# Performance work log

Hardware: AMD Instinct MI355X
Metric: run time of the kernel (lower is better)

Reference implementation:

```python
import jax, jax.numpy as jnp
import numpy as np

V = 131072        # vocab size = number of leaves (power of 2)
D = 17            # tree depth = log2(V)
B = 16384
E = 128


def setup_inputs() -> dict:
    key = jax.random.key(0)
    k1, k2, k3 = jax.random.split(key, 3)
    embeddings = jax.random.normal(k1, (B, E), dtype=jnp.float32)
    word_idx = jax.random.randint(k2, (B,), 0, V)
    # one Linear(E, 1) per internal node of the complete binary tree: V-1 internal nodes
    W = jax.random.normal(k3, (V - 1, E), dtype=jnp.float32) * (1.0 / np.sqrt(E))
    b = jnp.zeros((V - 1,), dtype=jnp.float32)
    return {"embeddings": embeddings, "word_idx": word_idx, "W": W, "b": b}


def _paths(word_idx):
    # Heap layout: leaf for word w is at index V-1+w; parent(i) = (i-1)//2.
    # Left child (2p+1, odd index) subtree holds the smaller words -> target 1.
    node = word_idx + (V - 1)
    nodes, dirs = [], []
    for _ in range(D):  # fixed small depth loop, unrolled by jit
        parent = (node - 1) // 2
        nodes.append(parent)
        dirs.append(node % 2)  # 1 iff we came from the left child
        node = parent
    return jnp.stack(nodes, axis=1), jnp.stack(dirs, axis=1)  # [B, D], [B, D]


def reference(embeddings, word_idx, W, b):
    nodes, dirs = _paths(word_idx)                 # int paths, leaf -> root
    Wn = W[nodes]                                  # [B, D, E] gather (memory-bound)
    bn = b[nodes]                                  # [B, D]
    s = jnp.einsum('bde,be->bd', Wn, embeddings) + bn   # per-node logit
    t = dirs.astype(s.dtype)                       # target: 1 = went left
    # numerically-stable BCE-with-logits, elementwise (matches per-node F.bce_with_logits on scalar)
    bce = jnp.maximum(s, 0.0) - s * t + jnp.log1p(jnp.exp(-jnp.abs(s)))
    return jnp.sum(bce) / embeddings.shape[0]
```

## Files before the change

kernel.cpp:

```cpp
#include <hip/hip_runtime.h>
#include <math.h>

constexpr int V = 131072;
constexpr int D = 17;
constexpr int B = 16384;
constexpr int E = 128;

constexpr int PAIRS = B * D;
constexpr int BLK   = 256;
constexpr int NBLK  = PAIRS / BLK;

__global__ __launch_bounds__(256) void hsm_pairs(
    const float* __restrict__ emb,
    const int*   __restrict__ widx,
    const float* __restrict__ W,
    const float* __restrict__ bias,
    float*       __restrict__ partial)
{
    const int tid = blockIdx.x * BLK + threadIdx.x;
    const int b   = tid / D;
    const int d   = tid - b * D;

    const int   j0   = widx[b] + V;
    const int   jc   = j0 >> d;
    const int   node = (jc >> 1) - 1;
    const float t    = (float)(1 - (jc & 1));

    const float4* er = (const float4*)(emb + (size_t)b    * E);
    const float4* wr = (const float4*)(W   + (size_t)node * E);

    float a0 = 0.f, a1 = 0.f, a2 = 0.f, a3 = 0.f;
    #pragma unroll
    for (int i = 0; i < E / 16; ++i) {
        float4 e0 = er[i*4+0], e1 = er[i*4+1], e2 = er[i*4+2], e3 = er[i*4+3];
        float4 w0 = wr[i*4+0], w1 = wr[i*4+1], w2 = wr[i*4+2], w3 = wr[i*4+3];
        a0 = fmaf(e0.x, w0.x, fmaf(e0.y, w0.y, fmaf(e0.z, w0.z, fmaf(e0.w, w0.w, a0))));
        a1 = fmaf(e1.x, w1.x, fmaf(e1.y, w1.y, fmaf(e1.z, w1.z, fmaf(e1.w, w1.w, a1))));
        a2 = fmaf(e2.x, w2.x, fmaf(e2.y, w2.y, fmaf(e2.z, w2.z, fmaf(e2.w, w2.w, a2))));
        a3 = fmaf(e3.x, w3.x, fmaf(e3.y, w3.y, fmaf(e3.z, w3.z, fmaf(e3.w, w3.w, a3))));
    }
    const float s = (a0 + a1) + (a2 + a3) + bias[node];

    float loss = fmaxf(s, 0.0f) - s * t + log1pf(expf(-fabsf(s)));

    #pragma unroll
    for (int off = 32; off >= 1; off >>= 1)
        loss += __shfl_xor(loss, off, 64);

    __shared__ float red[BLK / 64];
    const int lane = threadIdx.x & 63, wid = threadIdx.x >> 6;
    if (lane == 0) red[wid] = loss;
    __syncthreads();
    if (threadIdx.x == 0)
        partial[blockIdx.x] = (red[0] + red[1]) + (red[2] + red[3]);
}

__global__ __launch_bounds__(256) void hsm_reduce(
    const float* __restrict__ partial,
    float*       __restrict__ out)
{
    float s = 0.0f;
    for (int i = threadIdx.x; i < NBLK; i += 256) s += partial[i];
    #pragma unroll
    for (int off = 32; off >= 1; off >>= 1)
        s += __shfl_xor(s, off, 64);

    __shared__ float red[4];
    const int lane = threadIdx.x & 63, wid = threadIdx.x >> 6;
    if (lane == 0) red[wid] = s;
    __syncthreads();
    if (threadIdx.x == 0)
        out[0] = ((red[0] + red[1]) + (red[2] + red[3])) * (1.0f / (float)B);
}

extern "C" void kernel_launch(void* const* d_in, const int* in_sizes, int n_in,
                              void* d_out, int out_size, void* d_ws, size_t ws_size,
                              hipStream_t stream) {
    const float* emb  = (const float*)d_in[0];
    const int*   widx = (const int*)  d_in[1];
    const float* W    = (const float*)d_in[2];
    const float* bias = (const float*)d_in[3];
    float* out     = (float*)d_out;
    float* partial = (float*)d_ws;

    hsm_pairs<<<NBLK, BLK, 0, stream>>>(emb, widx, W, bias, partial);
    hsm_reduce<<<1, 256, 0, stream>>>(partial, out);
}
```

Before: 128.4 us.

## Assign 16 lanes per sample and loop over tree depth with shuffle reduction

Replaces the one-thread-per-(sample,node) mapping with 16 lanes cooperating on each sample's 128-wide dot products. Each group loads the embedding row once and walks all 17 ancestor nodes, reducing each dot product with xor shuffles. Weight-row loads become coalesced across lanes instead of strided per thread, and embedding reads are no longer repeated 17 times. It also switches to fast __logf/__expf intrinsics, which may slightly change numerical accuracy.

```diff
diff --git a/kernel.cpp b/kernel.cpp
--- a/kernel.cpp
+++ b/kernel.cpp
@@ -6,49 +6,62 @@
 constexpr int B = 16384;
 constexpr int E = 128;
 
-constexpr int PAIRS = B * D;
-constexpr int BLK   = 256;
-constexpr int NBLK  = PAIRS / BLK;
+constexpr int LPG  = 16;
+constexpr int SPB  = 16;
+constexpr int NBLK = B / SPB;
 
-__global__ __launch_bounds__(256) void hsm_pairs(
+__global__ __launch_bounds__(256) void hsm_main(
     const float* __restrict__ emb,
     const int*   __restrict__ widx,
     const float* __restrict__ W,
     const float* __restrict__ bias,
     float*       __restrict__ partial)
 {
-    const int tid = blockIdx.x * BLK + threadIdx.x;
-    const int b   = tid / D;
-    const int d   = tid - b * D;
+    const int lane = threadIdx.x & 63;
+    const int wid  = threadIdx.x >> 6;
+    const int g    = lane >> 4;
+    const int l    = lane & 15;
+    const int b    = blockIdx.x * SPB + wid * 4 + g;
 
-    const int   j0   = widx[b] + V;
-    const int   jc   = j0 >> d;
-    const int   node = (jc >> 1) - 1;
-    const float t    = (float)(1 - (jc & 1));
+    const float4* er = (const float4*)(emb + (size_t)b * E);
+    const float4 e0 = er[l];
+    const float4 e1 = er[l + LPG];
 
-    const float4* er = (const float4*)(emb + (size_t)b    * E);
-    const float4* wr = (const float4*)(W   + (size_t)node * E);
+    const int j0 = widx[b] + V;
 
-    float a0 = 0.f, a1 = 0.f, a2 = 0.f, a3 = 0.f;
+    float loss = 0.0f;
     #pragma unroll
-    for (int i = 0; i < E / 16; ++i) {
-        float4 e0 = er[i*4+0], e1 = er[i*4+1], e2 = er[i*4+2], e3 = er[i*4+3];
-        float4 w0 = wr[i*4+0], w1 = wr[i*4+1], w2 = wr[i*4+2], w3 = wr[i*4+3];
-        a0 = fmaf(e0.x, w0.x, fmaf(e0.y, w0.y, fmaf(e0.z, w0.z, fmaf(e0.w, w0.w, a0))));
-        a1 = fmaf(e1.x, w1.x, fmaf(e1.y, w1.y, fmaf(e1.z, w1.z, fmaf(e1.w, w1.w, a1))));
-        a2 = fmaf(e2.x, w2.x, fmaf(e2.y, w2.y, fmaf(e2.z, w2.z, fmaf(e2.w, w2.w, a2))));
-        a3 = fmaf(e3.x, w3.x, fmaf(e3.y, w3.y, fmaf(e3.z, w3.z, fmaf(e3.w, w3.w, a3))));
+    for (int d = 0; d < D; ++d) {
+        const int   jc   = j0 >> d;
+        const int   node = (jc >> 1) - 1;
+        const float t    = (float)(1 - (jc & 1));
+
+        const float4* wr = (const float4*)(W + (size_t)node * E);
+        const float4 w0 = wr[l];
+        const float4 w1 = wr[l + LPG];
+
+        float p;
+        p = fmaf(e0.x, w0.x, e0.y * w0.y);
+        p = fmaf(e0.z, w0.z, p);
+        p = fmaf(e0.w, w0.w, p);
+        p = fmaf(e1.x, w1.x, p);
+        p = fmaf(e1.y, w1.y, p);
+        p = fmaf(e1.z, w1.z, p);
+        p = fmaf(e1.w, w1.w, p);
+
+        p += __shfl_xor(p, 1, 64);
+        p += __shfl_xor(p, 2, 64);
+        p += __shfl_xor(p, 4, 64);
+        p += __shfl_xor(p, 8, 64);
+
+        const float s = p + bias[node];
+        loss += fmaxf(s, 0.0f) - s * t + __logf(1.0f + __expf(-fabsf(s)));
     }
-    const float s = (a0 + a1) + (a2 + a3) + bias[node];
 
-    float loss = fmaxf(s, 0.0f) - s * t + log1pf(expf(-fabsf(s)));
+    loss += __shfl_xor(loss, 16, 64);
+    loss += __shfl_xor(loss, 32, 64);
 
-    #pragma unroll
-    for (int off = 32; off >= 1; off >>= 1)
-        loss += __shfl_xor(loss, off, 64);
-
-    __shared__ float red[BLK / 64];
-    const int lane = threadIdx.x & 63, wid = threadIdx.x >> 6;
+    __shared__ float red[4];
     if (lane == 0) red[wid] = loss;
     __syncthreads();
     if (threadIdx.x == 0)
@@ -83,6 +96,6 @@
     float* out     = (float*)d_out;
     float* partial = (float*)d_ws;
 
-    hsm_pairs<<<NBLK, BLK, 0, stream>>>(emb, widx, W, bias, partial);
+    hsm_main<<<NBLK, 256, 0, stream>>>(emb, widx, W, bias, partial);
     hsm_reduce<<<1, 256, 0, stream>>>(partial, out);
 }
```

New measurement: 107.8 us, median of 3. 16.0% less time.
